# Kernel optimization log

Hardware: AMD Instinct MI355X
Metric: run time of the kernel (lower is better)

## Reference

```python
import jax, jax.numpy as jnp
import numpy as np
from jax import lax

B, T, D, I, K = 16, 2048, 512, 1024, 31

def setup_inputs() -> dict:
    key = jax.random.key(0)
    ks = jax.random.split(key, 5)
    x = jax.random.normal(ks[0], (B, T, D), dtype=jnp.float32)
    ln_g = jnp.ones((D,), jnp.float32)
    ln_b = jnp.zeros((D,), jnp.float32)
    w1 = jax.random.normal(ks[1], (2 * I, D), dtype=jnp.float32) * 0.02
    b1 = jnp.zeros((2 * I,), jnp.float32)
    dw = jax.random.normal(ks[2], (I, 1, K), dtype=jnp.float32) * 0.1
    dwb = jnp.zeros((I,), jnp.float32)
    alpha = jnp.full((I,), 0.25, jnp.float32)  # PReLU default init
    w2 = jax.random.normal(ks[3], (D, I), dtype=jnp.float32) * 0.02
    b2 = jnp.zeros((D,), jnp.float32)
    return {"x": x, "ln_g": ln_g, "ln_b": ln_b, "w1": w1, "b1": b1,
            "dw": dw, "dwb": dwb, "alpha": alpha, "w2": w2, "b2": b2}

def reference(x, ln_g, ln_b, w1, b1, dw, dwb, alpha, w2, b2):
    # LayerNorm over last dim
    mu = jnp.mean(x, axis=-1, keepdims=True)
    var = jnp.mean(jnp.square(x - mu), axis=-1, keepdims=True)
    xn = (x - mu) * lax.rsqrt(var + 1e-5) * ln_g + ln_b
    # pointwise conv D -> 2I (1x1 conv == GEMM over channels)
    h = jnp.einsum('btd,ed->bte', xn, w1) + b1            # [B,T,2I]
    a, g = jnp.split(h, 2, axis=-1)                       # chunk on channel dim
    u = a * jax.nn.silu(g)                                # SwiGLU [B,T,I]
    # depthwise conv, kernel 31, same padding 15
    uc = jnp.transpose(u, (0, 2, 1))                      # [B,I,T]
    pad = K // 2
    v = lax.conv_general_dilated(uc, dw, window_strides=(1,),
                                 padding=[(pad, pad)],
                                 dimension_numbers=('NCH', 'OIH', 'NCH'),
                                 feature_group_count=I)
    v = v + dwb[None, :, None]
    # PReLU per channel
    v = jnp.where(v > 0, v, alpha[None, :, None] * v)
    # pointwise conv I -> D, then back to [B,T,D]
    out = jnp.einsum('bct,dc->btd', v, w2) + b2
    return out
```

## Files before the change

### kernel.cpp

```cpp
#include <hip/hip_runtime.h>
#include <hip/hip_bf16.h>
#include <stdint.h>

#define B_  16
#define T_  2048
#define D_  512
#define I_  1024
#define K_  31
#define M_  (B_ * T_)

typedef __attribute__((ext_vector_type(8))) __bf16 bf16x8;
typedef __attribute__((ext_vector_type(4))) float  f32x4;

__device__ __forceinline__ unsigned short f2bf(float f) {
    union { float f; uint32_t u; } v; v.f = f;
    uint32_t u = v.u;
    uint32_t r = (u + 0x7FFFu + ((u >> 16) & 1u)) >> 16;
    return (unsigned short)r;
}
__device__ __forceinline__ float bf2f(unsigned short h) {
    union { uint32_t u; float f; } v; v.u = ((uint32_t)h) << 16;
    return v.f;
}

__device__ __forceinline__ void gload_lds16(const void* g, void* l) {
    __builtin_amdgcn_global_load_lds(
        (const __attribute__((address_space(1))) unsigned int*)g,
        (__attribute__((address_space(3))) unsigned int*)l, 16, 0, 0);
}

__global__ __launch_bounds__(256) void prep_weights(
    const float* __restrict__ w1, const float* __restrict__ w2,
    unsigned short* __restrict__ w1b, unsigned short* __restrict__ w2b)
{
    int i = blockIdx.x * 256 + threadIdx.x;
    const int n1 = 2 * I_ * D_;
    const int n2 = D_ * I_;
    if (i < n1) w1b[i] = f2bf(w1[i]);
    if (i < n2) w2b[i] = f2bf(w2[i]);
}

__global__ __launch_bounds__(256) void ln_kernel(
    const float* __restrict__ x, const float* __restrict__ gam,
    const float* __restrict__ bet, unsigned short* __restrict__ xn)
{
    int row  = blockIdx.x * 4 + (threadIdx.x >> 6);
    int lane = threadIdx.x & 63;
    const float* xr = x + (size_t)row * D_ + lane * 8;
    float4 a0 = *(const float4*)xr;
    float4 a1 = *(const float4*)(xr + 4);
    float xs[8] = {a0.x, a0.y, a0.z, a0.w, a1.x, a1.y, a1.z, a1.w};

    float s = xs[0]+xs[1]+xs[2]+xs[3]+xs[4]+xs[5]+xs[6]+xs[7];
    #pragma unroll
    for (int off = 32; off; off >>= 1) s += __shfl_xor(s, off);
    float mu = s * (1.0f / D_);

    float q = 0.f;
    #pragma unroll
    for (int j = 0; j < 8; ++j) { float d = xs[j] - mu; q += d * d; }
    #pragma unroll
    for (int off = 32; off; off >>= 1) q += __shfl_xor(q, off);
    float rstd = rsqrtf(q * (1.0f / D_) + 1e-5f);

    float4 g0 = *(const float4*)(gam + lane * 8);
    float4 g1 = *(const float4*)(gam + lane * 8 + 4);
    float4 e0 = *(const float4*)(bet + lane * 8);
    float4 e1 = *(const float4*)(bet + lane * 8 + 4);
    float gs[8] = {g0.x, g0.y, g0.z, g0.w, g1.x, g1.y, g1.z, g1.w};
    float bs[8] = {e0.x, e0.y, e0.z, e0.w, e1.x, e1.y, e1.z, e1.w};

    unsigned short o[8];
    #pragma unroll
    for (int j = 0; j < 8; ++j) o[j] = f2bf((xs[j] - mu) * rstd * gs[j] + bs[j]);
    uint4 pk;
    pk.x = (uint32_t)o[0] | ((uint32_t)o[1] << 16);
    pk.y = (uint32_t)o[2] | ((uint32_t)o[3] << 16);
    pk.z = (uint32_t)o[4] | ((uint32_t)o[5] << 16);
    pk.w = (uint32_t)o[6] | ((uint32_t)o[7] << 16);
    *(uint4*)(xn + (size_t)row * D_ + lane * 8) = pk;
}


#define VMCNT(n) asm volatile("s_waitcnt vmcnt(" #n ")" ::: "memory")

#define RD(base, idx) (*(const bf16x8*)(lds + (base) + (idx) * 2048))
#define MF(m, n, a, b) \
    acc[m][n] = __builtin_amdgcn_mfma_f32_16x16x32_bf16(a, b, acc[m][n], 0, 0, 0)
#define MFQ(MB, x0, x1, x2, x3, c0, c1, c2, c3) do { \
    MF(MB+0,0,x0,c0); MF(MB+0,1,x0,c1); MF(MB+0,2,x0,c2); MF(MB+0,3,x0,c3); \
    MF(MB+1,0,x1,c0); MF(MB+1,1,x1,c1); MF(MB+1,2,x1,c2); MF(MB+1,3,x1,c3); \
    MF(MB+2,0,x2,c0); MF(MB+2,1,x2,c1); MF(MB+2,2,x2,c2); MF(MB+2,3,x2,c3); \
    MF(MB+3,0,x3,c0); MF(MB+3,1,x3,c1); MF(MB+3,2,x3,c2); MF(MB+3,3,x3,c3); \
} while (0)

#define ISSUE_A(j, c) do { \
    gload_lds16(agA[j], lds + (c) * 65536 + tid * 16 + (j) * 8192); \
    agA[j] += 64; } while (0)
#define ISSUE_B(j, c) do { \
    gload_lds16(agB[j], lds + (c) * 65536 + 32768 + tid * 16 + (j) * 8192); \
    agB[j] += 64; } while (0)
#define ISSUE6(c) do { ISSUE_B(0,c); ISSUE_B(1,c); ISSUE_B(2,c); ISSUE_B(3,c); \
                       ISSUE_A(0,c); ISSUE_A(2,c); } while (0)
#define ISSUE2(c) do { ISSUE_A(1,c); ISSUE_A(3,c); } while (0)

#define LGKM_SCHED() do { \
    asm volatile("s_waitcnt lgkmcnt(0)" ::: "memory"); \
    __builtin_amdgcn_sched_barrier(0); } while (0)

#define KTILE2(CUR, NXT, DOISS) do { \
    bf16x8 b0,b1,b2,b3, x0,x1,x2,x3; \
    b0 = RD(bB0[CUR],0); b1 = RD(bB0[CUR],1); b2 = RD(bB0[CUR],2); b3 = RD(bB0[CUR],3); \
    x0 = RD(bA0[CUR],0); x1 = RD(bA0[CUR],1); x2 = RD(bA0[CUR],2); x3 = RD(bA0[CUR],3); \
    if (DOISS) { ISSUE6(NXT); } \
    __builtin_amdgcn_s_setprio(1); \
    MFQ(0, x0,x1,x2,x3, b0,b1,b2,b3); \
    __builtin_amdgcn_s_setprio(0); \
    LGKM_SCHED(); \
    if (DOISS) { VMCNT(6); } else { VMCNT(0); } \
    __builtin_amdgcn_s_barrier(); \
    x0 = RD(bA0[CUR],4); x1 = RD(bA0[CUR],5); x2 = RD(bA0[CUR],6); x3 = RD(bA0[CUR],7); \
    if (DOISS) { ISSUE2(NXT); } \
    __builtin_amdgcn_s_setprio(1); \
    MFQ(4, x0,x1,x2,x3, b0,b1,b2,b3); \
    __builtin_amdgcn_s_setprio(0); \
    b0 = RD(bB1[CUR],0); b1 = RD(bB1[CUR],1); b2 = RD(bB1[CUR],2); b3 = RD(bB1[CUR],3); \
    x0 = RD(bA1[CUR],0); x1 = RD(bA1[CUR],1); x2 = RD(bA1[CUR],2); x3 = RD(bA1[CUR],3); \
    __builtin_amdgcn_s_setprio(1); \
    MFQ(0, x0,x1,x2,x3, b0,b1,b2,b3); \
    __builtin_amdgcn_s_setprio(0); \
    x0 = RD(bA1[CUR],4); x1 = RD(bA1[CUR],5); x2 = RD(bA1[CUR],6); x3 = RD(bA1[CUR],7); \
    __builtin_amdgcn_s_setprio(1); \
    MFQ(4, x0,x1,x2,x3, b0,b1,b2,b3); \
    __builtin_amdgcn_s_setprio(0); \
    LGKM_SCHED(); \
    if (DOISS) { VMCNT(2); } \
    __builtin_amdgcn_s_barrier(); \
} while (0)

__global__ __launch_bounds__(512, 2) void gemm1_kernel(
    const unsigned short* __restrict__ xn,
    const unsigned short* __restrict__ w1b,
    const float* __restrict__ b1,
    unsigned short* __restrict__ u)
{
    __shared__ __align__(16) unsigned char lds[131072];
    const int tid  = threadIdx.x;
    const int lane = tid & 63;
    const int wv   = tid >> 6;
    const int wm   = wv >> 2;
    const int wn   = wv & 3;

    const int bid = blockIdx.x;
    const int sw  = (bid & 7) * 128 + (bid >> 3);
    const int jb  = sw & 7;
    const int m0  = (sw >> 3) * 256;

    const unsigned short* agA[4];
    const unsigned short* agB[4];
    {
        const int srow = tid >> 3;
        const int scb  = tid & 7;
        #pragma unroll
        for (int j = 0; j < 4; ++j) {
            int row = j * 64 + srow;
            int kk  = (scb ^ (row & 7)) * 8;
            agA[j] = xn + (size_t)(m0 + row) * D_ + kk;
            int chl  = ((row >> 5) << 4) + (row & 15);
            int wrow = ((row & 16) ? 1024 : 0) + jb * 128 + chl;
            agB[j] = w1b + (size_t)wrow * D_ + kk;
        }
    }

    const int l15 = lane & 15;
    const unsigned kq  = (unsigned)((lane >> 4) << 4);
    const unsigned swx = (unsigned)((l15 & 7) << 4);
    const unsigned rA  = (unsigned)(wm * 128 + l15) * 128;
    const unsigned rB  = 32768u + (unsigned)(wn * 64 + l15) * 128;
    const unsigned bA0[2] = {rA + (kq ^ swx),          rA + (kq ^ swx) + 65536u};
    const unsigned bA1[2] = {rA + ((64u + kq) ^ swx),  rA + ((64u + kq) ^ swx) + 65536u};
    const unsigned bB0[2] = {rB + (kq ^ swx),          rB + (kq ^ swx) + 65536u};
    const unsigned bB1[2] = {rB + ((64u + kq) ^ swx),  rB + ((64u + kq) ^ swx) + 65536u};

    f32x4 acc[8][4];
    #pragma unroll
    for (int i = 0; i < 8; ++i)
        #pragma unroll
        for (int n = 0; n < 4; ++n) acc[i][n] = (f32x4){0.f, 0.f, 0.f, 0.f};

    ISSUE6(0); ISSUE2(0);
    VMCNT(2);
    __builtin_amdgcn_s_barrier();

    #pragma unroll 1
    for (int h = 0; h < 3; ++h) {
        KTILE2(0, 1, true);
        KTILE2(1, 0, true);
    }
    KTILE2(0, 1, true);
    KTILE2(1, 0, false);

    const int rQ = (lane >> 4) * 4;
    #pragma unroll
    for (int p = 0; p < 2; ++p) {
        int ch = jb * 128 + wn * 32 + p * 16 + l15;
        float ba = b1[ch];
        float bg = b1[1024 + ch];
        #pragma unroll
        for (int mf = 0; mf < 8; ++mf) {
            #pragma unroll
            for (int r = 0; r < 4; ++r) {
                float a = acc[mf][2 * p][r] + ba;
                float g = acc[mf][2 * p + 1][r] + bg;
                float sg = g * __builtin_amdgcn_rcpf(1.0f + __expf(-g));
                int row = m0 + wm * 128 + mf * 16 + rQ + r;
                u[(size_t)row * I_ + ch] = f2bf(a * sg);
            }
        }
    }
}

__global__ __launch_bounds__(256) void dwconv_kernel(
    const unsigned short* __restrict__ u, const float* __restrict__ dw,
    const float* __restrict__ dwb, const float* __restrict__ alpha,
    unsigned short* __restrict__ v)
{
    __shared__ __align__(16) unsigned short su[286][64];
    const int tid     = threadIdx.x;
    const int c0      = blockIdx.y * 64;
    const int b       = blockIdx.z;
    const int tile_t0 = blockIdx.x * 256;

    #pragma unroll
    for (int it = 0; it < 9; ++it) {
        int r = it * 32 + (tid >> 3);
        if (r < 286) {
            int tt = tile_t0 - 15 + r;
            int cc = (tid & 7) * 8;
            uint4 val = {0u, 0u, 0u, 0u};
            if (tt >= 0 && tt < T_)
                val = *(const uint4*)(u + ((size_t)b * T_ + tt) * I_ + c0 + cc);
            *(uint4*)(&su[r][cc]) = val;
        }
    }
    __syncthreads();

    const int c  = tid & 63;
    const int tb = (tid >> 6) * 64;

    float dwk[K_];
    #pragma unroll
    for (int k = 0; k < K_; ++k) dwk[k] = dw[(c0 + c) * K_ + k];
    const float bia = dwb[c0 + c], al = alpha[c0 + c];

    unsigned short* vb = v + ((size_t)b * T_ + tile_t0 + tb) * I_ + c0 + c;

    #pragma unroll
    for (int chk = 0; chk < 4; ++chk) {
        float w[46];
        #pragma unroll
        for (int j = 0; j < 46; ++j)
            w[j] = bf2f(su[tb + chk * 16 + j][c]);
        #pragma unroll
        for (int i = 0; i < 16; ++i) {
            float acc = bia;
            #pragma unroll
            for (int k = 0; k < K_; ++k) acc += w[i + k] * dwk[k];
            float o = acc > 0.f ? acc : al * acc;
            vb[(size_t)(chk * 16 + i) * I_] = f2bf(o);
        }
    }
}

__global__ __launch_bounds__(512, 2) void gemm2_kernel(
    const unsigned short* __restrict__ v,
    const unsigned short* __restrict__ w2b,
    const float* __restrict__ b2,
    float* __restrict__ out)
{
    __shared__ __align__(16) unsigned char lds[131072];
    const int tid  = threadIdx.x;
    const int lane = tid & 63;
    const int wv   = tid >> 6;
    const int wm   = wv >> 2;
    const int wn   = wv & 3;

    const int bid = blockIdx.x;
    const int sw  = (bid & 7) * 32 + (bid >> 3);
    const int n0  = (sw & 1) * 256;
    const int m0  = (sw >> 1) * 256;

    const unsigned short* agA[4];
    const unsigned short* agB[4];
    {
        const int srow = tid >> 3;
        const int scb  = tid & 7;
        #pragma unroll
        for (int j = 0; j < 4; ++j) {
            int row = j * 64 + srow;
            int kk  = (scb ^ (row & 7)) * 8;
            agA[j] = v   + (size_t)(m0 + row) * I_ + kk;
            agB[j] = w2b + (size_t)(n0 + row) * I_ + kk;
        }
    }

    const int l15 = lane & 15;
    const unsigned kq  = (unsigned)((lane >> 4) << 4);
    const unsigned swx = (unsigned)((l15 & 7) << 4);
    const unsigned rA  = (unsigned)(wm * 128 + l15) * 128;
    const unsigned rB  = 32768u + (unsigned)(wn * 64 + l15) * 128;
    const unsigned bA0[2] = {rA + (kq ^ swx),          rA + (kq ^ swx) + 65536u};
    const unsigned bA1[2] = {rA + ((64u + kq) ^ swx),  rA + ((64u + kq) ^ swx) + 65536u};
    const unsigned bB0[2] = {rB + (kq ^ swx),          rB + (kq ^ swx) + 65536u};
    const unsigned bB1[2] = {rB + ((64u + kq) ^ swx),  rB + ((64u + kq) ^ swx) + 65536u};

    f32x4 acc[8][4];
    #pragma unroll
    for (int i = 0; i < 8; ++i)
        #pragma unroll
        for (int n = 0; n < 4; ++n) acc[i][n] = (f32x4){0.f, 0.f, 0.f, 0.f};

    ISSUE6(0); ISSUE2(0);
    VMCNT(2);
    __builtin_amdgcn_s_barrier();

    #pragma unroll 1
    for (int h = 0; h < 7; ++h) {
        KTILE2(0, 1, true);
        KTILE2(1, 0, true);
    }
    KTILE2(0, 1, true);
    KTILE2(1, 0, false);

    const int rQ = (lane >> 4) * 4;
    #pragma unroll
    for (int nf = 0; nf < 4; ++nf) {
        int col = n0 + wn * 64 + nf * 16 + l15;
        float bb = b2[col];
        #pragma unroll
        for (int mf = 0; mf < 8; ++mf) {
            #pragma unroll
            for (int r = 0; r < 4; ++r) {
                int row = m0 + wm * 128 + mf * 16 + rQ + r;
                out[(size_t)row * D_ + col] = acc[mf][nf][r] + bb;
            }
        }
    }
}

extern "C" void kernel_launch(void* const* d_in, const int* in_sizes, int n_in,
                              void* d_out, int out_size, void* d_ws, size_t ws_size,
                              hipStream_t stream) {
    const float* x     = (const float*)d_in[0];
    const float* ln_g  = (const float*)d_in[1];
    const float* ln_b  = (const float*)d_in[2];
    const float* w1    = (const float*)d_in[3];
    const float* b1    = (const float*)d_in[4];
    const float* dw    = (const float*)d_in[5];
    const float* dwb   = (const float*)d_in[6];
    const float* alpha = (const float*)d_in[7];
    const float* w2    = (const float*)d_in[8];
    const float* b2    = (const float*)d_in[9];
    float* out = (float*)d_out;

    char* ws = (char*)d_ws;
    unsigned short* xn  = (unsigned short*)(ws);
    unsigned short* u   = (unsigned short*)(ws + 33554432);
    unsigned short* v   = (unsigned short*)(ws + 100663296);
    unsigned short* w1b = (unsigned short*)(ws + 167772160);
    unsigned short* w2b = (unsigned short*)(ws + 169869312);

    prep_weights<<<4096, 256, 0, stream>>>(w1, w2, w1b, w2b);
    ln_kernel<<<M_ / 4, 256, 0, stream>>>(x, ln_g, ln_b, xn);
    gemm1_kernel<<<(M_ / 256) * (I_ / 128), 512, 0, stream>>>(xn, w1b, b1, u);
    dim3 gc(T_ / 256, I_ / 64, B_);
    dwconv_kernel<<<gc, 256, 0, stream>>>(u, dw, dwb, alpha, v);
    gemm2_kernel<<<256, 512, 0, stream>>>(v, w2b, b2, out);
}
```

Baseline: 193.0 us.

## Switch GEMMs to 4-stage LDS ring with K=32 tiles

Replaces the double-buffered K=64 LDS pipeline in both GEMM kernels with a four-slot ring of K=32 tiles, prefetching three tiles ahead and using a new 4-slot XOR swizzle. Each stage does one LDS read burst, 32 MFMAs and a single barrier, instead of the previous split half-tile schedule. The goal is deeper global-load latency hiding at the same LDS footprint, at the cost of twice as many barriers per K and smaller per-load transfers.

New measurement: 204.9 us. +6.1%, slower.

```diff
diff --git a/kernel.cpp b/kernel.cpp
--- a/kernel.cpp
+++ b/kernel.cpp
@@ -84,57 +84,40 @@
 
 #define VMCNT(n) asm volatile("s_waitcnt vmcnt(" #n ")" ::: "memory")
 
-#define RD(base, idx) (*(const bf16x8*)(lds + (base) + (idx) * 2048))
+#define RD4(c, base, idx) (*(const bf16x8*)(lds + (c) * 32768 + (base) + (idx) * 1024))
 #define MF(m, n, a, b) \
     acc[m][n] = __builtin_amdgcn_mfma_f32_16x16x32_bf16(a, b, acc[m][n], 0, 0, 0)
-#define MFQ(MB, x0, x1, x2, x3, c0, c1, c2, c3) do { \
-    MF(MB+0,0,x0,c0); MF(MB+0,1,x0,c1); MF(MB+0,2,x0,c2); MF(MB+0,3,x0,c3); \
-    MF(MB+1,0,x1,c0); MF(MB+1,1,x1,c1); MF(MB+1,2,x1,c2); MF(MB+1,3,x1,c3); \
-    MF(MB+2,0,x2,c0); MF(MB+2,1,x2,c1); MF(MB+2,2,x2,c2); MF(MB+2,3,x2,c3); \
-    MF(MB+3,0,x3,c0); MF(MB+3,1,x3,c1); MF(MB+3,2,x3,c2); MF(MB+3,3,x3,c3); \
+
+#define ISSUE4(c) do { \
+    gload_lds16(agA[0], lds + (c) * 32768 +         tid * 16); agA[0] += 32; \
+    gload_lds16(agA[1], lds + (c) * 32768 +  8192 + tid * 16); agA[1] += 32; \
+    gload_lds16(agB[0], lds + (c) * 32768 + 16384 + tid * 16); agB[0] += 32; \
+    gload_lds16(agB[1], lds + (c) * 32768 + 24576 + tid * 16); agB[1] += 32; \
 } while (0)
-
-#define ISSUE_A(j, c) do { \
-    gload_lds16(agA[j], lds + (c) * 65536 + tid * 16 + (j) * 8192); \
-    agA[j] += 64; } while (0)
-#define ISSUE_B(j, c) do { \
-    gload_lds16(agB[j], lds + (c) * 65536 + 32768 + tid * 16 + (j) * 8192); \
-    agB[j] += 64; } while (0)
-#define ISSUE6(c) do { ISSUE_B(0,c); ISSUE_B(1,c); ISSUE_B(2,c); ISSUE_B(3,c); \
-                       ISSUE_A(0,c); ISSUE_A(2,c); } while (0)
-#define ISSUE2(c) do { ISSUE_A(1,c); ISSUE_A(3,c); } while (0)
 
 #define LGKM_SCHED() do { \
     asm volatile("s_waitcnt lgkmcnt(0)" ::: "memory"); \
     __builtin_amdgcn_sched_barrier(0); } while (0)
 
-#define KTILE2(CUR, NXT, DOISS) do { \
-    bf16x8 b0,b1,b2,b3, x0,x1,x2,x3; \
-    b0 = RD(bB0[CUR],0); b1 = RD(bB0[CUR],1); b2 = RD(bB0[CUR],2); b3 = RD(bB0[CUR],3); \
-    x0 = RD(bA0[CUR],0); x1 = RD(bA0[CUR],1); x2 = RD(bA0[CUR],2); x3 = RD(bA0[CUR],3); \
-    if (DOISS) { ISSUE6(NXT); } \
+#define KT(CUR, DOISS, VM) do { \
+    bf16x8 b0,b1,b2,b3, a0,a1,a2,a3,a4,a5,a6,a7; \
+    b0 = RD4(CUR, rB, 0); b1 = RD4(CUR, rB, 1); b2 = RD4(CUR, rB, 2); b3 = RD4(CUR, rB, 3); \
+    a0 = RD4(CUR, rA, 0); a1 = RD4(CUR, rA, 1); a2 = RD4(CUR, rA, 2); a3 = RD4(CUR, rA, 3); \
+    a4 = RD4(CUR, rA, 4); a5 = RD4(CUR, rA, 5); a6 = RD4(CUR, rA, 6); a7 = RD4(CUR, rA, 7); \
+    if (DOISS) { ISSUE4((CUR + 3) & 3); } \
     __builtin_amdgcn_s_setprio(1); \
-    MFQ(0, x0,x1,x2,x3, b0,b1,b2,b3); \
+    MF(0,0,a0,b0); MF(0,1,a0,b1); MF(0,2,a0,b2); MF(0,3,a0,b3); \
+    MF(1,0,a1,b0); MF(1,1,a1,b1); MF(1,2,a1,b2); MF(1,3,a1,b3); \
+    MF(2,0,a2,b0); MF(2,1,a2,b1); MF(2,2,a2,b2); MF(2,3,a2,b3); \
+    MF(3,0,a3,b0); MF(3,1,a3,b1); MF(3,2,a3,b2); MF(3,3,a3,b3); \
+    MF(4,0,a4,b0); MF(4,1,a4,b1); MF(4,2,a4,b2); MF(4,3,a4,b3); \
+    MF(5,0,a5,b0); MF(5,1,a5,b1); MF(5,2,a5,b2); MF(5,3,a5,b3); \
+    MF(6,0,a6,b0); MF(6,1,a6,b1); MF(6,2,a6,b2); MF(6,3,a6,b3); \
+    MF(7,0,a7,b0); MF(7,1,a7,b1); MF(7,2,a7,b2); MF(7,3,a7,b3); \
     __builtin_amdgcn_s_setprio(0); \
     LGKM_SCHED(); \
-    if (DOISS) { VMCNT(6); } else { VMCNT(0); } \
-    __builtin_amdgcn_s_barrier(); \
-    x0 = RD(bA0[CUR],4); x1 = RD(bA0[CUR],5); x2 = RD(bA0[CUR],6); x3 = RD(bA0[CUR],7); \
-    if (DOISS) { ISSUE2(NXT); } \
-    __builtin_amdgcn_s_setprio(1); \
-    MFQ(4, x0,x1,x2,x3, b0,b1,b2,b3); \
-    __builtin_amdgcn_s_setprio(0); \
-    b0 = RD(bB1[CUR],0); b1 = RD(bB1[CUR],1); b2 = RD(bB1[CUR],2); b3 = RD(bB1[CUR],3); \
-    x0 = RD(bA1[CUR],0); x1 = RD(bA1[CUR],1); x2 = RD(bA1[CUR],2); x3 = RD(bA1[CUR],3); \
-    __builtin_amdgcn_s_setprio(1); \
-    MFQ(0, x0,x1,x2,x3, b0,b1,b2,b3); \
-    __builtin_amdgcn_s_setprio(0); \
-    x0 = RD(bA1[CUR],4); x1 = RD(bA1[CUR],5); x2 = RD(bA1[CUR],6); x3 = RD(bA1[CUR],7); \
-    __builtin_amdgcn_s_setprio(1); \
-    MFQ(4, x0,x1,x2,x3, b0,b1,b2,b3); \
-    __builtin_amdgcn_s_setprio(0); \
-    LGKM_SCHED(); \
-    if (DOISS) { VMCNT(2); } \
+    if ((VM) == 8) { VMCNT(8); } else if ((VM) == 4) { VMCNT(4); } \
+    else if ((VM) == 0) { VMCNT(0); } \
     __builtin_amdgcn_s_barrier(); \
 } while (0)
 
@@ -156,15 +139,15 @@
     const int jb  = sw & 7;
     const int m0  = (sw >> 3) * 256;
 
-    const unsigned short* agA[4];
-    const unsigned short* agB[4];
+    const unsigned short* agA[2];
+    const unsigned short* agB[2];
     {
-        const int srow = tid >> 3;
-        const int scb  = tid & 7;
-        #pragma unroll
-        for (int j = 0; j < 4; ++j) {
-            int row = j * 64 + srow;
-            int kk  = (scb ^ (row & 7)) * 8;
+        const int srow = tid >> 2;
+        const int scb  = tid & 3;
+        #pragma unroll
+        for (int j = 0; j < 2; ++j) {
+            int row = j * 128 + srow;
+            int kk  = (scb ^ (row & 3)) * 8;
             agA[j] = xn + (size_t)(m0 + row) * D_ + kk;
             int chl  = ((row >> 5) << 4) + (row & 15);
             int wrow = ((row & 16) ? 1024 : 0) + jb * 128 + chl;
@@ -173,14 +156,9 @@
     }
 
     const int l15 = lane & 15;
-    const unsigned kq  = (unsigned)((lane >> 4) << 4);
-    const unsigned swx = (unsigned)((l15 & 7) << 4);
-    const unsigned rA  = (unsigned)(wm * 128 + l15) * 128;
-    const unsigned rB  = 32768u + (unsigned)(wn * 64 + l15) * 128;
-    const unsigned bA0[2] = {rA + (kq ^ swx),          rA + (kq ^ swx) + 65536u};
-    const unsigned bA1[2] = {rA + ((64u + kq) ^ swx),  rA + ((64u + kq) ^ swx) + 65536u};
-    const unsigned bB0[2] = {rB + (kq ^ swx),          rB + (kq ^ swx) + 65536u};
-    const unsigned bB1[2] = {rB + ((64u + kq) ^ swx),  rB + ((64u + kq) ^ swx) + 65536u};
+    const unsigned slotx = (unsigned)(((lane >> 4) ^ (l15 & 3)) << 4);
+    const unsigned rA = (unsigned)(wm * 128 + l15) * 64 + slotx;
+    const unsigned rB = 16384u + (unsigned)(wn * 64 + l15) * 64 + slotx;
 
     f32x4 acc[8][4];
     #pragma unroll
@@ -188,17 +166,18 @@
         #pragma unroll
         for (int n = 0; n < 4; ++n) acc[i][n] = (f32x4){0.f, 0.f, 0.f, 0.f};
 
-    ISSUE6(0); ISSUE2(0);
-    VMCNT(2);
+    ISSUE4(0); ISSUE4(1); ISSUE4(2);
+    VMCNT(8);
     __builtin_amdgcn_s_barrier();
 
     #pragma unroll 1
     for (int h = 0; h < 3; ++h) {
-        KTILE2(0, 1, true);
-        KTILE2(1, 0, true);
-    }
-    KTILE2(0, 1, true);
-    KTILE2(1, 0, false);
+        KT(0, true, 8); KT(1, true, 8); KT(2, true, 8); KT(3, true, 8);
+    }
+    KT(0, true,  8);
+    KT(1, false, 4);
+    KT(2, false, 0);
+    KT(3, false, -1);
 
     const int rQ = (lane >> 4) * 4;
     #pragma unroll
@@ -290,29 +269,24 @@
     const int n0  = (sw & 1) * 256;
     const int m0  = (sw >> 1) * 256;
 
-    const unsigned short* agA[4];
-    const unsigned short* agB[4];
+    const unsigned short* agA[2];
+    const unsigned short* agB[2];
     {
-        const int srow = tid >> 3;
-        const int scb  = tid & 7;
-        #pragma unroll
-        for (int j = 0; j < 4; ++j) {
-            int row = j * 64 + srow;
-            int kk  = (scb ^ (row & 7)) * 8;
+        const int srow = tid >> 2;
+        const int scb  = tid & 3;
+        #pragma unroll
+        for (int j = 0; j < 2; ++j) {
+            int row = j * 128 + srow;
+            int kk  = (scb ^ (row & 3)) * 8;
             agA[j] = v   + (size_t)(m0 + row) * I_ + kk;
             agB[j] = w2b + (size_t)(n0 + row) * I_ + kk;
         }
     }
 
     const int l15 = lane & 15;
-    const unsigned kq  = (unsigned)((lane >> 4) << 4);
-    const unsigned swx = (unsigned)((l15 & 7) << 4);
-    const unsigned rA  = (unsigned)(wm * 128 + l15) * 128;
-    const unsigned rB  = 32768u + (unsigned)(wn * 64 + l15) * 128;
-    const unsigned bA0[2] = {rA + (kq ^ swx),          rA + (kq ^ swx) + 65536u};
-    const unsigned bA1[2] = {rA + ((64u + kq) ^ swx),  rA + ((64u + kq) ^ swx) + 65536u};
-    const unsigned bB0[2] = {rB + (kq ^ swx),          rB + (kq ^ swx) + 65536u};
-    const unsigned bB1[2] = {rB + ((64u + kq) ^ swx),  rB + ((64u + kq) ^ swx) + 65536u};
+    const unsigned slotx = (unsigned)(((lane >> 4) ^ (l15 & 3)) << 4);
+    const unsigned rA = (unsigned)(wm * 128 + l15) * 64 + slotx;
+    const unsigned rB = 16384u + (unsigned)(wn * 64 + l15) * 64 + slotx;
 
     f32x4 acc[8][4];
     #pragma unroll
@@ -320,17 +294,18 @@
         #pragma unroll
         for (int n = 0; n < 4; ++n) acc[i][n] = (f32x4){0.f, 0.f, 0.f, 0.f};
 
-    ISSUE6(0); ISSUE2(0);
-    VMCNT(2);
+    ISSUE4(0); ISSUE4(1); ISSUE4(2);
+    VMCNT(8);
     __builtin_amdgcn_s_barrier();
 
     #pragma unroll 1
     for (int h = 0; h < 7; ++h) {
-        KTILE2(0, 1, true);
-        KTILE2(1, 0, true);
-    }
-    KTILE2(0, 1, true);
-    KTILE2(1, 0, false);
+        KT(0, true, 8); KT(1, true, 8); KT(2, true, 8); KT(3, true, 8);
+    }
+    KT(0, true,  8);
+    KT(1, false, 4);
+    KT(2, false, 0);
+    KT(3, false, -1);
 
     const int rQ = (lane >> 4) * 4;
     #pragma unroll
```

## Restructure GEMM k-tile pipeline with staged lgkmcnt waits and single barrier

Applied to the files above, without the earlier changes.

Replaces the two-phase k-tile body, which had two barriers and a split global→LDS issue (6+2 loads), with one k-tile that issues all 16 LDS fragment reads up front. MFMA quads are gated by progressive lgkmcnt waits (12/8/4/0), and all 8 global loads are issued at once with a single vmcnt(0)+barrier per tile. The aim is to cut barrier count and let LDS reads overlap MFMA issue, in both GEMM kernels. In exchange it uses more VGPRs for the extra fragments, which risks pressure at launch_bounds(512,2). It also removes the earlier partial-wait overlap, since the next tile's loads now must fully land before the barrier.

Result: slower. 220.1 us (+14.0%).

```diff
diff --git a/kernel.cpp b/kernel.cpp
--- a/kernel.cpp
+++ b/kernel.cpp
@@ -83,6 +83,10 @@
 
 
 #define VMCNT(n) asm volatile("s_waitcnt vmcnt(" #n ")" ::: "memory")
+#define LGKM(n)  asm volatile("s_waitcnt lgkmcnt(" #n ")" ::: "memory")
+#define SCHB     __builtin_amdgcn_sched_barrier(0)
+#define PRIO1    __builtin_amdgcn_s_setprio(1)
+#define PRIO0    __builtin_amdgcn_s_setprio(0)
 
 #define RD(base, idx) (*(const bf16x8*)(lds + (base) + (idx) * 2048))
 #define MF(m, n, a, b) \
@@ -100,41 +104,23 @@
 #define ISSUE_B(j, c) do { \
     gload_lds16(agB[j], lds + (c) * 65536 + 32768 + tid * 16 + (j) * 8192); \
     agB[j] += 64; } while (0)
-#define ISSUE6(c) do { ISSUE_B(0,c); ISSUE_B(1,c); ISSUE_B(2,c); ISSUE_B(3,c); \
-                       ISSUE_A(0,c); ISSUE_A(2,c); } while (0)
-#define ISSUE2(c) do { ISSUE_A(1,c); ISSUE_A(3,c); } while (0)
-
-#define LGKM_SCHED() do { \
-    asm volatile("s_waitcnt lgkmcnt(0)" ::: "memory"); \
-    __builtin_amdgcn_sched_barrier(0); } while (0)
-
-#define KTILE2(CUR, NXT, DOISS) do { \
-    bf16x8 b0,b1,b2,b3, x0,x1,x2,x3; \
-    b0 = RD(bB0[CUR],0); b1 = RD(bB0[CUR],1); b2 = RD(bB0[CUR],2); b3 = RD(bB0[CUR],3); \
-    x0 = RD(bA0[CUR],0); x1 = RD(bA0[CUR],1); x2 = RD(bA0[CUR],2); x3 = RD(bA0[CUR],3); \
-    if (DOISS) { ISSUE6(NXT); } \
-    __builtin_amdgcn_s_setprio(1); \
-    MFQ(0, x0,x1,x2,x3, b0,b1,b2,b3); \
-    __builtin_amdgcn_s_setprio(0); \
-    LGKM_SCHED(); \
-    if (DOISS) { VMCNT(6); } else { VMCNT(0); } \
-    __builtin_amdgcn_s_barrier(); \
-    x0 = RD(bA0[CUR],4); x1 = RD(bA0[CUR],5); x2 = RD(bA0[CUR],6); x3 = RD(bA0[CUR],7); \
-    if (DOISS) { ISSUE2(NXT); } \
-    __builtin_amdgcn_s_setprio(1); \
-    MFQ(4, x0,x1,x2,x3, b0,b1,b2,b3); \
-    __builtin_amdgcn_s_setprio(0); \
-    b0 = RD(bB1[CUR],0); b1 = RD(bB1[CUR],1); b2 = RD(bB1[CUR],2); b3 = RD(bB1[CUR],3); \
-    x0 = RD(bA1[CUR],0); x1 = RD(bA1[CUR],1); x2 = RD(bA1[CUR],2); x3 = RD(bA1[CUR],3); \
-    __builtin_amdgcn_s_setprio(1); \
-    MFQ(0, x0,x1,x2,x3, b0,b1,b2,b3); \
-    __builtin_amdgcn_s_setprio(0); \
-    x0 = RD(bA1[CUR],4); x1 = RD(bA1[CUR],5); x2 = RD(bA1[CUR],6); x3 = RD(bA1[CUR],7); \
-    __builtin_amdgcn_s_setprio(1); \
-    MFQ(4, x0,x1,x2,x3, b0,b1,b2,b3); \
-    __builtin_amdgcn_s_setprio(0); \
-    LGKM_SCHED(); \
-    if (DOISS) { VMCNT(2); } \
+#define ISSUE8(c) do { ISSUE_B(0,c); ISSUE_B(1,c); ISSUE_B(2,c); ISSUE_B(3,c); \
+                       ISSUE_A(0,c); ISSUE_A(1,c); ISSUE_A(2,c); ISSUE_A(3,c); } while (0)
+
+#define KT8(CUR, NXT, DOISS) do { \
+    bf16x8 b00,b01,b02,b03, b10,b11,b12,b13, p0,p1,p2,p3, q0,q1,q2,q3, s0,s1,s2,s3; \
+    b00 = RD(bB0[CUR],0); b01 = RD(bB0[CUR],1); b02 = RD(bB0[CUR],2); b03 = RD(bB0[CUR],3); \
+    p0  = RD(bA0[CUR],0); p1  = RD(bA0[CUR],1); p2  = RD(bA0[CUR],2); p3  = RD(bA0[CUR],3); \
+    q0  = RD(bA0[CUR],4); q1  = RD(bA0[CUR],5); q2  = RD(bA0[CUR],6); q3  = RD(bA0[CUR],7); \
+    b10 = RD(bB1[CUR],0); b11 = RD(bB1[CUR],1); b12 = RD(bB1[CUR],2); b13 = RD(bB1[CUR],3); \
+    s0  = RD(bA1[CUR],0); s1  = RD(bA1[CUR],1); s2  = RD(bA1[CUR],2); s3  = RD(bA1[CUR],3); \
+    if (DOISS) { ISSUE8(NXT); } \
+    LGKM(12); SCHB; PRIO1; MFQ(0, p0,p1,p2,p3, b00,b01,b02,b03); PRIO0; \
+    LGKM(8);  SCHB; PRIO1; MFQ(4, q0,q1,q2,q3, b00,b01,b02,b03); PRIO0; \
+    q0 = RD(bA1[CUR],4); q1 = RD(bA1[CUR],5); q2 = RD(bA1[CUR],6); q3 = RD(bA1[CUR],7); \
+    LGKM(4);  SCHB; PRIO1; MFQ(0, s0,s1,s2,s3, b10,b11,b12,b13); PRIO0; \
+    LGKM(0);  SCHB; PRIO1; MFQ(4, q0,q1,q2,q3, b10,b11,b12,b13); PRIO0; \
+    if (DOISS) { VMCNT(0); } \
     __builtin_amdgcn_s_barrier(); \
 } while (0)
 
@@ -188,17 +174,17 @@
         #pragma unroll
         for (int n = 0; n < 4; ++n) acc[i][n] = (f32x4){0.f, 0.f, 0.f, 0.f};
 
-    ISSUE6(0); ISSUE2(0);
-    VMCNT(2);
+    ISSUE8(0);
+    VMCNT(0);
     __builtin_amdgcn_s_barrier();
 
     #pragma unroll 1
     for (int h = 0; h < 3; ++h) {
-        KTILE2(0, 1, true);
-        KTILE2(1, 0, true);
-    }
-    KTILE2(0, 1, true);
-    KTILE2(1, 0, false);
+        KT8(0, 1, true);
+        KT8(1, 0, true);
+    }
+    KT8(0, 1, true);
+    KT8(1, 0, false);
 
     const int rQ = (lane >> 4) * 4;
     #pragma unroll
@@ -320,17 +306,17 @@
         #pragma unroll
         for (int n = 0; n < 4; ++n) acc[i][n] = (f32x4){0.f, 0.f, 0.f, 0.f};
 
-    ISSUE6(0); ISSUE2(0);
-    VMCNT(2);
+    ISSUE8(0);
+    VMCNT(0);
     __builtin_amdgcn_s_barrier();
 
     #pragma unroll 1
     for (int h = 0; h < 7; ++h) {
-        KTILE2(0, 1, true);
-        KTILE2(1, 0, true);
-    }
-    KTILE2(0, 1, true);
-    KTILE2(1, 0, false);
+        KT8(0, 1, true);
+        KT8(1, 0, true);
+    }
+    KT8(0, 1, true);
+    KT8(1, 0, false);
 
     const int rQ = (lane >> 4) * 4;
     #pragma unroll
```
